# Kernel tuning notes

Hardware: AMD Instinct MI355X
Metric: run time of the kernel (lower is better)

## Reference

```python
import jax, jax.numpy as jnp
import numpy as np

B, T, F = 8192, 30, 16
H1, H2 = 64, 32


def _lstm(x, Wih, Whh, b):
    """PyTorch-convention LSTM (gate order i,f,g,o). x: [B,T,I] -> (ys [B,T,H], hT [B,H])."""
    H = Whh.shape[1]
    h0 = jnp.zeros((x.shape[0], H), x.dtype)

    def step(carry, xt):
        h, c = carry
        z = xt @ Wih.T + h @ Whh.T + b  # [B,4H]
        i, f, g, o = jnp.split(z, 4, axis=-1)
        c = jax.nn.sigmoid(f) * c + jax.nn.sigmoid(i) * jnp.tanh(g)
        h = jax.nn.sigmoid(o) * jnp.tanh(c)
        return (h, c), h

    (hT, _), ys = jax.lax.scan(step, (h0, h0), jnp.swapaxes(x, 0, 1))
    return jnp.swapaxes(ys, 0, 1), hT


def setup_inputs() -> dict:
    key = jax.random.key(0)
    ks = jax.random.split(key, 16)
    s = 0.1  # small init scale for numerical sanity
    return {
        "x": jax.random.normal(ks[0], (B, T, F), jnp.float32),
        "Wih1": jax.random.normal(ks[1], (4 * H1, F), jnp.float32) * s,
        "Whh1": jax.random.normal(ks[2], (4 * H1, H1), jnp.float32) * s,
        "b1": jax.random.normal(ks[3], (4 * H1,), jnp.float32) * s,
        "Wih2": jax.random.normal(ks[4], (4 * H2, H1), jnp.float32) * s,
        "Whh2": jax.random.normal(ks[5], (4 * H2, H2), jnp.float32) * s,
        "b2": jax.random.normal(ks[6], (4 * H2,), jnp.float32) * s,
        "Wih3": jax.random.normal(ks[7], (4 * H2, H2), jnp.float32) * s,
        "Whh3": jax.random.normal(ks[8], (4 * H2, H2), jnp.float32) * s,
        "b3": jax.random.normal(ks[9], (4 * H2,), jnp.float32) * s,
        "Wih4": jax.random.normal(ks[10], (4 * H1, H2), jnp.float32) * s,
        "Whh4": jax.random.normal(ks[11], (4 * H1, H1), jnp.float32) * s,
        "b4": jax.random.normal(ks[12], (4 * H1,), jnp.float32) * s,
        "Wout": jax.random.normal(ks[13], (F, H1), jnp.float32) * s,
        "bout": jax.random.normal(ks[14], (F,), jnp.float32) * s,
    }


def reference(x, Wih1, Whh1, b1, Wih2, Whh2, b2, Wih3, Whh3, b3, Wih4, Whh4, b4, Wout, bout):
    ys1, _ = _lstm(x, Wih1, Whh1, b1)          # encoder LSTM(64)
    _, latent = _lstm(ys1, Wih2, Whh2, b2)      # encoder LSTM(32) -> final hidden [B,32]
    repeated = jnp.broadcast_to(latent[:, None, :], (latent.shape[0], T, latent.shape[1]))
    ys3, _ = _lstm(repeated, Wih3, Whh3, b3)    # decoder LSTM(32)
    ys4, _ = _lstm(ys3, Wih4, Whh4, b4)         # decoder LSTM(64)
    return ys4 @ Wout.T + bout                  # [B,T,F]
```

## Files before the change

### kernel.cpp

```cpp
#include <hip/hip_runtime.h>


#define TT 30
#define FF 16
#define NT 768

typedef unsigned short u16t;
typedef __attribute__((ext_vector_type(8))) short short8;
typedef __attribute__((ext_vector_type(4))) short short4v;
typedef __attribute__((ext_vector_type(4))) float floatx4;

#define MFMA(a, b, c) __builtin_amdgcn_mfma_f32_16x16x32_bf16(a, b, c, 0, 0, 0)

#if __has_builtin(__builtin_amdgcn_exp2f)
#define EXP2(x) __builtin_amdgcn_exp2f(x)
#else
#define EXP2(x) exp2f(x)
#endif

template <int P> struct IC { static constexpr int v = P; };

__device__ __forceinline__ float rcpf(float v) { return __builtin_amdgcn_rcpf(v); }
__device__ __forceinline__ u16t f2bf(float f) {
  unsigned int u = __float_as_uint(f);
  u = (u + 0x7FFFu + ((u >> 16) & 1u)) >> 16;
  return (u16t)u;
}
__device__ __forceinline__ unsigned int pkbf(float a, float b) {
  unsigned int r;
  asm("v_cvt_pk_bf16_f32 %0, %1, %2" : "=v"(r) : "v"(a), "v"(b));
  return r;
}
__device__ __forceinline__ void barLDS() {
  asm volatile("s_waitcnt lgkmcnt(0)" ::: "memory");
  __builtin_amdgcn_s_barrier();
}
__device__ __forceinline__ short8 ldFragS(const float* p, float s) {
  const float4 lo = *(const float4*)p;
  const float4 hi = *(const float4*)(p + 4);
  short8 r;
  r[0] = (short)f2bf(lo.x * s); r[1] = (short)f2bf(lo.y * s);
  r[2] = (short)f2bf(lo.z * s); r[3] = (short)f2bf(lo.w * s);
  r[4] = (short)f2bf(hi.x * s); r[5] = (short)f2bf(hi.y * s);
  r[6] = (short)f2bf(hi.z * s); r[7] = (short)f2bf(hi.w * s);
  return r;
}
__device__ __forceinline__ float cellUp(const floatx4 acc, float& c) {
  float ei = EXP2(-acc[0]);
  float ef = EXP2(-acc[1]);
  float eg = EXP2(-acc[2]);
  float eo = EXP2(-acc[3]);
  float pig = (1.f + ei) * (1.f + eg);
  float pf  = 1.f + ef;
  float num = c * pig + (1.f - eg) * pf;
  c = num * rcpf(pf * pig);
  float ec = EXP2(-2.885390082f * c);
  return (1.f - ec) * rcpf((1.f + eo) * (1.f + ec));
}

__global__ __launch_bounds__(NT, 3) void lstm_ae_mfma12(
    const float* __restrict__ x,
    const float* __restrict__ Wih1, const float* __restrict__ Whh1, const float* __restrict__ b1,
    const float* __restrict__ Wih2, const float* __restrict__ Whh2, const float* __restrict__ b2,
    const float* __restrict__ Wih3, const float* __restrict__ Whh3, const float* __restrict__ b3,
    const float* __restrict__ Wih4, const float* __restrict__ Whh4, const float* __restrict__ b4,
    const float* __restrict__ Wout, const float* __restrict__ bout,
    float* __restrict__ out)
{
  __shared__ __align__(16) u16t xAll[32 * 968];
  __shared__ __align__(16) u16t aB[32 * 264];

  const int t = threadIdx.x;
  const int w = t >> 6, lane = t & 63;
  const int q = lane >> 4, n = lane & 15;
  const int q8 = q * 8;
  const int bBase = blockIdx.x * 32;
  const int nlo = n >> 2, ngt = n & 3;
  const bool isZ1 = (w < 8);
  const int hf = w & 1;
  const int jA = w >> 1;
  const int j2 = (w >> 1) - 4;
  const int rh = (n + 16 * hf) * 264;
  const int xh = (n + 16 * hf) * 968;

  const float L1 = 1.442695041f, L2 = 2.885390082f;
  const float sA = (ngt == 2) ? L2 : L1;

  for (int i = t; i < 32 * 264; i += NT) aB[i] = 0;
  {
    const float* xb = x + (size_t)bBase * (TT * FF);
    for (int i4 = t; i4 < 3840; i4 += NT) {
      int e = i4 * 4;
      int b = e / 480, r = e - b * 480;
      int stp = r >> 4, f = r & 15;
      float4 v = *(const float4*)&xb[e];
      short4v s4 = { (short)f2bf(v.x), (short)f2bf(v.y), (short)f2bf(v.z), (short)f2bf(v.w) };
      *(short4v*)&xAll[b * 968 + stp * 32 + f] = s4;
    }
    for (int i = t; i < 15360; i += NT) {
      int b = i / 480, r = i - b * 480;
      int stp = r >> 4, f = r & 15;
      xAll[b * 968 + stp * 32 + 16 + f] = 0;
    }
  }
  const short8 z8 = { 0, 0, 0, 0, 0, 0, 0, 0 };
  short8 wAf[4][3]; floatx4 biasA[4];
  if (isZ1) {
#pragma unroll
    for (int tt = 0; tt < 4; ++tt) {
      int T = jA + 4 * tt;
      int row = ngt * 64 + T * 4 + nlo;
      wAf[tt][0] = z8;
      if (q < 2) wAf[tt][0] = ldFragS(&Wih1[row * 16 + q8], sA);
      wAf[tt][1] = ldFragS(&Whh1[row * 64 + q8], sA);
      wAf[tt][2] = ldFragS(&Whh1[row * 64 + 32 + q8], sA);
#pragma unroll
      for (int r = 0; r < 4; ++r) biasA[tt][r] = b1[r * 64 + T * 4 + q] * (r == 2 ? L2 : L1);
    }
  } else {
#pragma unroll
    for (int tt = 0; tt < 4; ++tt) {
      int T = j2 + 2 * tt;
      int row = ngt * 32 + T * 4 + nlo;
      wAf[tt][0] = ldFragS(&Wih2[row * 64 + q8], sA);
      wAf[tt][1] = ldFragS(&Wih2[row * 64 + 32 + q8], sA);
      wAf[tt][2] = ldFragS(&Whh2[row * 32 + q8], sA);
#pragma unroll
      for (int r = 0; r < 4; ++r) biasA[tt][r] = b2[r * 32 + T * 4 + q] * (r == 2 ? L2 : L1);
    }
  }
  __syncthreads();

  float cA[4] = {0.f, 0.f, 0.f, 0.f};
  short8 bxN;
  float hv[4];

  if (isZ1) {
    const short8 bx0 = *(const short8*)&xAll[xh + q8];
#pragma unroll
    for (int tt = 0; tt < 4; ++tt) {
      floatx4 a = biasA[tt];
      a = MFMA(wAf[tt][0], bx0, a);
      hv[tt] = cellUp(a, cA[tt]);
    }
    unsigned int pk01 = pkbf(hv[0], hv[1]);
    unsigned int pk23 = pkbf(hv[2], hv[3]);
    aB[rh + (jA + 0) * 4 + q] = (u16t)pk01;
    aB[rh + (jA + 4) * 4 + q] = (u16t)(pk01 >> 16);
    aB[rh + (jA + 8) * 4 + q] = (u16t)pk23;
    aB[rh + (jA + 12) * 4 + q] = (u16t)(pk23 >> 16);
    bxN = *(const short8*)&xAll[xh + 32 + q8];
  }
  barLDS();

  auto stepA = [&](int st, auto pc) {
    constexpr int p = decltype(pc)::v;
    const short8 h1a = *(const short8*)&aB[rh + p * 64 + q8];
    const short8 h1b = *(const short8*)&aB[rh + p * 64 + 32 + q8];
    if (isZ1) {
#pragma unroll
      for (int tt = 0; tt < 4; ++tt) {
        floatx4 a = biasA[tt];
        a = MFMA(wAf[tt][0], bxN, a);
        a = MFMA(wAf[tt][1], h1a, a);
        a = MFMA(wAf[tt][2], h1b, a);
        hv[tt] = cellUp(a, cA[tt]);
      }
      unsigned int pk01 = pkbf(hv[0], hv[1]);
      unsigned int pk23 = pkbf(hv[2], hv[3]);
      aB[rh + (1 - p) * 64 + (jA + 0) * 4 + q] = (u16t)pk01;
      aB[rh + (1 - p) * 64 + (jA + 4) * 4 + q] = (u16t)(pk01 >> 16);
      aB[rh + (1 - p) * 64 + (jA + 8) * 4 + q] = (u16t)pk23;
      aB[rh + (1 - p) * 64 + (jA + 12) * 4 + q] = (u16t)(pk23 >> 16);
      const int nx = (st + 2 < TT) ? st + 2 : TT - 1;
      bxN = *(const short8*)&xAll[xh + nx * 32 + q8];
    } else {
      const short8 h2 = *(const short8*)&aB[rh + 128 + (1 - p) * 32 + q8];
#pragma unroll
      for (int tt = 0; tt < 4; ++tt) {
        floatx4 a = biasA[tt];
        a = MFMA(wAf[tt][0], h1a, a);
        a = MFMA(wAf[tt][1], h1b, a);
        a = MFMA(wAf[tt][2], h2, a);
        hv[tt] = cellUp(a, cA[tt]);
      }
      unsigned int pk01 = pkbf(hv[0], hv[1]);
      unsigned int pk23 = pkbf(hv[2], hv[3]);
      aB[rh + 128 + p * 32 + (j2 + 0) * 4 + q] = (u16t)pk01;
      aB[rh + 128 + p * 32 + (j2 + 2) * 4 + q] = (u16t)(pk01 >> 16);
      aB[rh + 128 + p * 32 + (j2 + 4) * 4 + q] = (u16t)pk23;
      aB[rh + 128 + p * 32 + (j2 + 6) * 4 + q] = (u16t)(pk23 >> 16);
    }
    barLDS();
  };
  for (int st = 0; st < 28; st += 2) { stepA(st, IC<0>{}); stepA(st + 1, IC<1>{}); }
  stepA(28, IC<0>{});
  if (!isZ1) {
    const short8 h1a = *(const short8*)&aB[rh + 64 + q8];
    const short8 h1b = *(const short8*)&aB[rh + 96 + q8];
    const short8 h2  = *(const short8*)&aB[rh + 128 + q8];
#pragma unroll
    for (int tt = 0; tt < 4; ++tt) {
      floatx4 a = biasA[tt];
      a = MFMA(wAf[tt][0], h1a, a);
      a = MFMA(wAf[tt][1], h1b, a);
      a = MFMA(wAf[tt][2], h2, a);
      hv[tt] = cellUp(a, cA[tt]);
    }
    unsigned int pk01 = pkbf(hv[0], hv[1]);
    unsigned int pk23 = pkbf(hv[2], hv[3]);
    aB[rh + 160 + (j2 + 0) * 4 + q] = (u16t)pk01;
    aB[rh + 160 + (j2 + 2) * 4 + q] = (u16t)(pk01 >> 16);
    aB[rh + 160 + (j2 + 4) * 4 + q] = (u16t)pk23;
    aB[rh + 160 + (j2 + 6) * 4 + q] = (u16t)(pk23 >> 16);
  }
  __syncthreads();

  short8 wBf[4][3]; floatx4 biasB[4];
  short8 wof[2]; floatx4 biasO;
  short8 w3h[4]; floatx4 acc3c[4];
  if (isZ1) {
#pragma unroll
    for (int tt = 0; tt < 4; ++tt) {
      int T = jA + 4 * tt;
      int row = ngt * 64 + T * 4 + nlo;
      wBf[tt][0] = ldFragS(&Wih4[row * 32 + q8], sA);
      wBf[tt][1] = ldFragS(&Whh4[row * 64 + q8], sA);
      wBf[tt][2] = ldFragS(&Whh4[row * 64 + 32 + q8], sA);
#pragma unroll
      for (int r = 0; r < 4; ++r) biasB[tt][r] = b4[r * 64 + T * 4 + q] * (r == 2 ? L2 : L1);
    }
    wof[0] = ldFragS(&Wout[n * 64 + q8], 1.f);
    wof[1] = ldFragS(&Wout[n * 64 + 32 + q8], 1.f);
    biasO = *(const floatx4*)&bout[q * 4];
  } else {
    const short8 blat = *(const short8*)&aB[rh + 160 + q8];
#pragma unroll
    for (int tt = 0; tt < 4; ++tt) {
      int T = j2 + 2 * tt;
      int row = ngt * 32 + T * 4 + nlo;
      const short8 w3i = ldFragS(&Wih3[row * 32 + q8], sA);
      w3h[tt] = ldFragS(&Whh3[row * 32 + q8], sA);
      floatx4 b3v;
#pragma unroll
      for (int r = 0; r < 4; ++r) b3v[r] = b3[r * 32 + T * 4 + q] * (r == 2 ? L2 : L1);
      acc3c[tt] = MFMA(w3i, blat, b3v);
    }
  }
  for (int i = t; i < 2048; i += NT) aB[(i >> 6) * 264 + 64 + (i & 63)] = 0;
  __syncthreads();

  float cB[4] = {0.f, 0.f, 0.f, 0.f};

  if (!isZ1) {
#pragma unroll
    for (int tt = 0; tt < 4; ++tt) hv[tt] = cellUp(acc3c[tt], cB[tt]);
    unsigned int pk01 = pkbf(hv[0], hv[1]);
    unsigned int pk23 = pkbf(hv[2], hv[3]);
    aB[rh + 192 + (j2 + 0) * 4 + q] = (u16t)pk01;
    aB[rh + 192 + (j2 + 2) * 4 + q] = (u16t)(pk01 >> 16);
    aB[rh + 192 + (j2 + 4) * 4 + q] = (u16t)pk23;
    aB[rh + 192 + (j2 + 6) * 4 + q] = (u16t)(pk23 >> 16);
  }
  barLDS();

  auto stepB = [&](int st, auto pc) {
    constexpr int p = decltype(pc)::v;
    const short8 h3 = *(const short8*)&aB[rh + 192 + p * 32 + q8];
    if (isZ1) {
      const short8 h4a = *(const short8*)&aB[rh + (1 - p) * 64 + q8];
      const short8 h4b = *(const short8*)&aB[rh + (1 - p) * 64 + 32 + q8];
#pragma unroll
      for (int tt = 0; tt < 4; ++tt) {
        floatx4 a = biasB[tt];
        a = MFMA(wBf[tt][0], h3, a);
        a = MFMA(wBf[tt][1], h4a, a);
        a = MFMA(wBf[tt][2], h4b, a);
        hv[tt] = cellUp(a, cB[tt]);
      }
      unsigned int pk01 = pkbf(hv[0], hv[1]);
      unsigned int pk23 = pkbf(hv[2], hv[3]);
      aB[rh + p * 64 + (jA + 0) * 4 + q] = (u16t)pk01;
      aB[rh + p * 64 + (jA + 4) * 4 + q] = (u16t)(pk01 >> 16);
      aB[rh + p * 64 + (jA + 8) * 4 + q] = (u16t)pk23;
      aB[rh + p * 64 + (jA + 12) * 4 + q] = (u16t)(pk23 >> 16);
      if (st > 0 && jA == ((st - 1) & 3)) {
        floatx4 y = biasO;
        y = MFMA(wof[0], h4a, y);
        y = MFMA(wof[1], h4b, y);
        *(floatx4*)&out[((size_t)(bBase + n + 16 * hf) * TT + (st - 1)) * FF + q * 4] = y;
      }
    } else {
#pragma unroll
      for (int tt = 0; tt < 4; ++tt) {
        floatx4 a = MFMA(w3h[tt], h3, acc3c[tt]);
        hv[tt] = cellUp(a, cB[tt]);
      }
      unsigned int pk01 = pkbf(hv[0], hv[1]);
      unsigned int pk23 = pkbf(hv[2], hv[3]);
      aB[rh + 192 + (1 - p) * 32 + (j2 + 0) * 4 + q] = (u16t)pk01;
      aB[rh + 192 + (1 - p) * 32 + (j2 + 2) * 4 + q] = (u16t)(pk01 >> 16);
      aB[rh + 192 + (1 - p) * 32 + (j2 + 4) * 4 + q] = (u16t)pk23;
      aB[rh + 192 + (1 - p) * 32 + (j2 + 6) * 4 + q] = (u16t)(pk23 >> 16);
    }
    barLDS();
  };
  for (int st = 0; st < 28; st += 2) { stepB(st, IC<0>{}); stepB(st + 1, IC<1>{}); }
  stepB(28, IC<0>{});
  if (isZ1) {
    const short8 h3  = *(const short8*)&aB[rh + 224 + q8];
    const short8 h4a = *(const short8*)&aB[rh + q8];
    const short8 h4b = *(const short8*)&aB[rh + 32 + q8];
#pragma unroll
    for (int tt = 0; tt < 4; ++tt) {
      floatx4 a = biasB[tt];
      a = MFMA(wBf[tt][0], h3, a);
      a = MFMA(wBf[tt][1], h4a, a);
      a = MFMA(wBf[tt][2], h4b, a);
      hv[tt] = cellUp(a, cB[tt]);
    }
    unsigned int pk01 = pkbf(hv[0], hv[1]);
    unsigned int pk23 = pkbf(hv[2], hv[3]);
    aB[rh + 64 + (jA + 0) * 4 + q] = (u16t)pk01;
    aB[rh + 64 + (jA + 4) * 4 + q] = (u16t)(pk01 >> 16);
    aB[rh + 64 + (jA + 8) * 4 + q] = (u16t)pk23;
    aB[rh + 64 + (jA + 12) * 4 + q] = (u16t)(pk23 >> 16);
    if (jA == 0) {
      floatx4 y = biasO;
      y = MFMA(wof[0], h4a, y);
      y = MFMA(wof[1], h4b, y);
      *(floatx4*)&out[((size_t)(bBase + n + 16 * hf) * TT + 28) * FF + q * 4] = y;
    }
  }
  barLDS();
  if (isZ1 && jA == 1) {
    const short8 ba = *(const short8*)&aB[rh + 64 + q8];
    const short8 bb = *(const short8*)&aB[rh + 96 + q8];
    floatx4 y = biasO;
    y = MFMA(wof[0], ba, y);
    y = MFMA(wof[1], bb, y);
    *(floatx4*)&out[((size_t)(bBase + n + 16 * hf) * TT + 29) * FF + q * 4] = y;
  }
}

extern "C" void kernel_launch(void* const* d_in, const int* in_sizes, int n_in,
                              void* d_out, int out_size, void* d_ws, size_t ws_size,
                              hipStream_t stream) {
  const float* x    = (const float*)d_in[0];
  const float* Wih1 = (const float*)d_in[1];
  const float* Whh1 = (const float*)d_in[2];
  const float* b1   = (const float*)d_in[3];
  const float* Wih2 = (const float*)d_in[4];
  const float* Whh2 = (const float*)d_in[5];
  const float* b2   = (const float*)d_in[6];
  const float* Wih3 = (const float*)d_in[7];
  const float* Whh3 = (const float*)d_in[8];
  const float* b3   = (const float*)d_in[9];
  const float* Wih4 = (const float*)d_in[10];
  const float* Whh4 = (const float*)d_in[11];
  const float* b4   = (const float*)d_in[12];
  const float* Wout = (const float*)d_in[13];
  const float* bout = (const float*)d_in[14];
  float* out = (float*)d_out;

  const int B = in_sizes[0] / (TT * FF);
  dim3 grid(B / 32), block(NT);
  lstm_ae_mfma12<<<grid, block, 0, stream>>>(
      x, Wih1, Whh1, b1, Wih2, Whh2, b2, Wih3, Whh3, b3,
      Wih4, Whh4, b4, Wout, bout, out);
}
```

Before: 161.4 us.

## Replace block-wide barriers with per-half LDS flag synchronization between LSTM waves

Swaps each per-timestep block barrier for LDS flag counters. A wave spins on only the flags of the producer waves it depends on, within its own 16-row batch half. Wave-to-work assignment is regrouped so each half's layer-1/layer-2 (and layer-3/layer-4) waves form independent groups that can drift out of lockstep. The aim is to cut barrier stalls and let the two stacked layers pipeline across timesteps. It adds spin-polling overhead and relies on LDS ordering with volatile flags, which carries a memory-ordering risk. Double buffers can race if a consumer lags more than one step behind.

```diff
diff --git a/kernel.cpp b/kernel.cpp
--- a/kernel.cpp
+++ b/kernel.cpp
@@ -30,10 +30,6 @@
   unsigned int r;
   asm("v_cvt_pk_bf16_f32 %0, %1, %2" : "=v"(r) : "v"(a), "v"(b));
   return r;
-}
-__device__ __forceinline__ void barLDS() {
-  asm volatile("s_waitcnt lgkmcnt(0)" ::: "memory");
-  __builtin_amdgcn_s_barrier();
 }
 __device__ __forceinline__ short8 ldFragS(const float* p, float s) {
   const float4 lo = *(const float4*)p;
@@ -57,8 +53,26 @@
   float ec = EXP2(-2.885390082f * c);
   return (1.f - ec) * rcpf((1.f + eo) * (1.f + ec));
 }
-
-__global__ __launch_bounds__(NT, 3) void lstm_ae_mfma12(
+__device__ __forceinline__ void wait4(const int* f, int tgt) {
+  for (;;) {
+    int a = *(volatile const int*)&f[0];
+    int b = *(volatile const int*)&f[1];
+    int c = *(volatile const int*)&f[2];
+    int d = *(volatile const int*)&f[3];
+    if (a >= tgt && b >= tgt && c >= tgt && d >= tgt) break;
+    __builtin_amdgcn_s_sleep(1);
+  }
+}
+__device__ __forceinline__ void wait2(const int* f, int tgt) {
+  for (;;) {
+    int a = *(volatile const int*)&f[0];
+    int b = *(volatile const int*)&f[1];
+    if (a >= tgt && b >= tgt) break;
+    __builtin_amdgcn_s_sleep(1);
+  }
+}
+
+__global__ __launch_bounds__(NT, 3) void lstm_ae_mfma13(
     const float* __restrict__ x,
     const float* __restrict__ Wih1, const float* __restrict__ Whh1, const float* __restrict__ b1,
     const float* __restrict__ Wih2, const float* __restrict__ Whh2, const float* __restrict__ b2,
@@ -69,6 +83,7 @@
 {
   __shared__ __align__(16) u16t xAll[32 * 968];
   __shared__ __align__(16) u16t aB[32 * 264];
+  __shared__ int flg[16];
 
   const int t = threadIdx.x;
   const int w = t >> 6, lane = t & 63;
@@ -77,16 +92,18 @@
   const int bBase = blockIdx.x * 32;
   const int nlo = n >> 2, ngt = n & 3;
   const bool isZ1 = (w < 8);
-  const int hf = w & 1;
-  const int jA = w >> 1;
-  const int j2 = (w >> 1) - 4;
+  const int hf = isZ1 ? ((w >> 2) & 1) : (w & 1);
+  const int jA = w & 3;
+  const int j2 = (w >> 1) & 1;
   const int rh = (n + 16 * hf) * 264;
   const int xh = (n + 16 * hf) * 968;
+  const int myFlag = isZ1 ? (hf * 4 + jA) : (8 + hf * 2 + j2);
 
   const float L1 = 1.442695041f, L2 = 2.885390082f;
   const float sA = (ngt == 2) ? L2 : L1;
 
   for (int i = t; i < 32 * 264; i += NT) aB[i] = 0;
+  for (int i = t; i < 16; i += NT) flg[i] = -1;
   {
     const float* xb = x + (size_t)bBase * (TT * FF);
     for (int i4 = t; i4 < 3840; i4 += NT) {
@@ -132,73 +149,41 @@
   __syncthreads();
 
   float cA[4] = {0.f, 0.f, 0.f, 0.f};
-  short8 bxN;
   float hv[4];
 
-  if (isZ1) {
-    const short8 bx0 = *(const short8*)&xAll[xh + q8];
+  auto stepA1 = [&](int s, auto pc) {
+    constexpr int P = pc.v;
+    wait4(&flg[hf * 4], s - 1);
+    wait2(&flg[8 + hf * 2], s - 2);
+    __builtin_amdgcn_sched_barrier(0);
+    const short8 bx  = *(const short8*)&xAll[xh + s * 32 + q8];
+    const short8 h1a = *(const short8*)&aB[rh + (1 - P) * 64 + q8];
+    const short8 h1b = *(const short8*)&aB[rh + (1 - P) * 64 + 32 + q8];
 #pragma unroll
     for (int tt = 0; tt < 4; ++tt) {
       floatx4 a = biasA[tt];
-      a = MFMA(wAf[tt][0], bx0, a);
+      a = MFMA(wAf[tt][0], bx, a);
+      a = MFMA(wAf[tt][1], h1a, a);
+      a = MFMA(wAf[tt][2], h1b, a);
       hv[tt] = cellUp(a, cA[tt]);
     }
     unsigned int pk01 = pkbf(hv[0], hv[1]);
     unsigned int pk23 = pkbf(hv[2], hv[3]);
-    aB[rh + (jA + 0) * 4 + q] = (u16t)pk01;
-    aB[rh + (jA + 4) * 4 + q] = (u16t)(pk01 >> 16);
-    aB[rh + (jA + 8) * 4 + q] = (u16t)pk23;
-    aB[rh + (jA + 12) * 4 + q] = (u16t)(pk23 >> 16);
-    bxN = *(const short8*)&xAll[xh + 32 + q8];
-  }
-  barLDS();
-
-  auto stepA = [&](int st, auto pc) {
-    constexpr int p = decltype(pc)::v;
-    const short8 h1a = *(const short8*)&aB[rh + p * 64 + q8];
-    const short8 h1b = *(const short8*)&aB[rh + p * 64 + 32 + q8];
-    if (isZ1) {
-#pragma unroll
-      for (int tt = 0; tt < 4; ++tt) {
-        floatx4 a = biasA[tt];
-        a = MFMA(wAf[tt][0], bxN, a);
-        a = MFMA(wAf[tt][1], h1a, a);
-        a = MFMA(wAf[tt][2], h1b, a);
-        hv[tt] = cellUp(a, cA[tt]);
-      }
-      unsigned int pk01 = pkbf(hv[0], hv[1]);
-      unsigned int pk23 = pkbf(hv[2], hv[3]);
-      aB[rh + (1 - p) * 64 + (jA + 0) * 4 + q] = (u16t)pk01;
-      aB[rh + (1 - p) * 64 + (jA + 4) * 4 + q] = (u16t)(pk01 >> 16);
-      aB[rh + (1 - p) * 64 + (jA + 8) * 4 + q] = (u16t)pk23;
-      aB[rh + (1 - p) * 64 + (jA + 12) * 4 + q] = (u16t)(pk23 >> 16);
-      const int nx = (st + 2 < TT) ? st + 2 : TT - 1;
-      bxN = *(const short8*)&xAll[xh + nx * 32 + q8];
-    } else {
-      const short8 h2 = *(const short8*)&aB[rh + 128 + (1 - p) * 32 + q8];
-#pragma unroll
-      for (int tt = 0; tt < 4; ++tt) {
-        floatx4 a = biasA[tt];
-        a = MFMA(wAf[tt][0], h1a, a);
-        a = MFMA(wAf[tt][1], h1b, a);
-        a = MFMA(wAf[tt][2], h2, a);
-        hv[tt] = cellUp(a, cA[tt]);
-      }
-      unsigned int pk01 = pkbf(hv[0], hv[1]);
-      unsigned int pk23 = pkbf(hv[2], hv[3]);
-      aB[rh + 128 + p * 32 + (j2 + 0) * 4 + q] = (u16t)pk01;
-      aB[rh + 128 + p * 32 + (j2 + 2) * 4 + q] = (u16t)(pk01 >> 16);
-      aB[rh + 128 + p * 32 + (j2 + 4) * 4 + q] = (u16t)pk23;
-      aB[rh + 128 + p * 32 + (j2 + 6) * 4 + q] = (u16t)(pk23 >> 16);
-    }
-    barLDS();
+    aB[rh + P * 64 + (jA + 0) * 4 + q] = (u16t)pk01;
+    aB[rh + P * 64 + (jA + 4) * 4 + q] = (u16t)(pk01 >> 16);
+    aB[rh + P * 64 + (jA + 8) * 4 + q] = (u16t)pk23;
+    aB[rh + P * 64 + (jA + 12) * 4 + q] = (u16t)(pk23 >> 16);
+    asm volatile("s_waitcnt lgkmcnt(0)" ::: "memory");
+    *(volatile int*)&flg[myFlag] = s;
   };
-  for (int st = 0; st < 28; st += 2) { stepA(st, IC<0>{}); stepA(st + 1, IC<1>{}); }
-  stepA(28, IC<0>{});
-  if (!isZ1) {
-    const short8 h1a = *(const short8*)&aB[rh + 64 + q8];
-    const short8 h1b = *(const short8*)&aB[rh + 96 + q8];
-    const short8 h2  = *(const short8*)&aB[rh + 128 + q8];
+  auto stepA2 = [&](int s, auto pc) {
+    constexpr int P = pc.v;
+    wait4(&flg[hf * 4], s);
+    wait2(&flg[8 + hf * 2], s - 1);
+    __builtin_amdgcn_sched_barrier(0);
+    const short8 h1a = *(const short8*)&aB[rh + P * 64 + q8];
+    const short8 h1b = *(const short8*)&aB[rh + P * 64 + 32 + q8];
+    const short8 h2  = *(const short8*)&aB[rh + 128 + (1 - P) * 32 + q8];
 #pragma unroll
     for (int tt = 0; tt < 4; ++tt) {
       floatx4 a = biasA[tt];
@@ -209,13 +194,23 @@
     }
     unsigned int pk01 = pkbf(hv[0], hv[1]);
     unsigned int pk23 = pkbf(hv[2], hv[3]);
-    aB[rh + 160 + (j2 + 0) * 4 + q] = (u16t)pk01;
-    aB[rh + 160 + (j2 + 2) * 4 + q] = (u16t)(pk01 >> 16);
-    aB[rh + 160 + (j2 + 4) * 4 + q] = (u16t)pk23;
-    aB[rh + 160 + (j2 + 6) * 4 + q] = (u16t)(pk23 >> 16);
+    const int base = (s == TT - 1) ? (rh + 160) : (rh + 128 + P * 32);
+    aB[base + (j2 + 0) * 4 + q] = (u16t)pk01;
+    aB[base + (j2 + 2) * 4 + q] = (u16t)(pk01 >> 16);
+    aB[base + (j2 + 4) * 4 + q] = (u16t)pk23;
+    aB[base + (j2 + 6) * 4 + q] = (u16t)(pk23 >> 16);
+    asm volatile("s_waitcnt lgkmcnt(0)" ::: "memory");
+    *(volatile int*)&flg[myFlag] = s;
+  };
+  if (isZ1) {
+    for (int s = 0; s < TT; s += 2) { stepA1(s, IC<0>{}); stepA1(s + 1, IC<1>{}); }
+  } else {
+    for (int s = 0; s < TT; s += 2) { stepA2(s, IC<0>{}); stepA2(s + 1, IC<1>{}); }
   }
   __syncthreads();
 
+  for (int i = t; i < 16; i += NT) flg[i] = -1;
+  for (int i = t; i < 2048; i += NT) aB[(i >> 6) * 264 + 64 + (i & 63)] = 0;
   short8 wBf[4][3]; floatx4 biasB[4];
   short8 wof[2]; floatx4 biasO;
   short8 w3h[4]; floatx4 acc3c[4];
@@ -247,70 +242,18 @@
       acc3c[tt] = MFMA(w3i, blat, b3v);
     }
   }
-  for (int i = t; i < 2048; i += NT) aB[(i >> 6) * 264 + 64 + (i & 63)] = 0;
   __syncthreads();
 
   float cB[4] = {0.f, 0.f, 0.f, 0.f};
 
-  if (!isZ1) {
-#pragma unroll
-    for (int tt = 0; tt < 4; ++tt) hv[tt] = cellUp(acc3c[tt], cB[tt]);
-    unsigned int pk01 = pkbf(hv[0], hv[1]);
-    unsigned int pk23 = pkbf(hv[2], hv[3]);
-    aB[rh + 192 + (j2 + 0) * 4 + q] = (u16t)pk01;
-    aB[rh + 192 + (j2 + 2) * 4 + q] = (u16t)(pk01 >> 16);
-    aB[rh + 192 + (j2 + 4) * 4 + q] = (u16t)pk23;
-    aB[rh + 192 + (j2 + 6) * 4 + q] = (u16t)(pk23 >> 16);
-  }
-  barLDS();
-
-  auto stepB = [&](int st, auto pc) {
-    constexpr int p = decltype(pc)::v;
-    const short8 h3 = *(const short8*)&aB[rh + 192 + p * 32 + q8];
-    if (isZ1) {
-      const short8 h4a = *(const short8*)&aB[rh + (1 - p) * 64 + q8];
-      const short8 h4b = *(const short8*)&aB[rh + (1 - p) * 64 + 32 + q8];
-#pragma unroll
-      for (int tt = 0; tt < 4; ++tt) {
-        floatx4 a = biasB[tt];
-        a = MFMA(wBf[tt][0], h3, a);
-        a = MFMA(wBf[tt][1], h4a, a);
-        a = MFMA(wBf[tt][2], h4b, a);
-        hv[tt] = cellUp(a, cB[tt]);
-      }
-      unsigned int pk01 = pkbf(hv[0], hv[1]);
-      unsigned int pk23 = pkbf(hv[2], hv[3]);
-      aB[rh + p * 64 + (jA + 0) * 4 + q] = (u16t)pk01;
-      aB[rh + p * 64 + (jA + 4) * 4 + q] = (u16t)(pk01 >> 16);
-      aB[rh + p * 64 + (jA + 8) * 4 + q] = (u16t)pk23;
-      aB[rh + p * 64 + (jA + 12) * 4 + q] = (u16t)(pk23 >> 16);
-      if (st > 0 && jA == ((st - 1) & 3)) {
-        floatx4 y = biasO;
-        y = MFMA(wof[0], h4a, y);
-        y = MFMA(wof[1], h4b, y);
-        *(floatx4*)&out[((size_t)(bBase + n + 16 * hf) * TT + (st - 1)) * FF + q * 4] = y;
-      }
-    } else {
-#pragma unroll
-      for (int tt = 0; tt < 4; ++tt) {
-        floatx4 a = MFMA(w3h[tt], h3, acc3c[tt]);
-        hv[tt] = cellUp(a, cB[tt]);
-      }
-      unsigned int pk01 = pkbf(hv[0], hv[1]);
-      unsigned int pk23 = pkbf(hv[2], hv[3]);
-      aB[rh + 192 + (1 - p) * 32 + (j2 + 0) * 4 + q] = (u16t)pk01;
-      aB[rh + 192 + (1 - p) * 32 + (j2 + 2) * 4 + q] = (u16t)(pk01 >> 16);
-      aB[rh + 192 + (1 - p) * 32 + (j2 + 4) * 4 + q] = (u16t)pk23;
-      aB[rh + 192 + (1 - p) * 32 + (j2 + 6) * 4 + q] = (u16t)(pk23 >> 16);
-    }
-    barLDS();
-  };
-  for (int st = 0; st < 28; st += 2) { stepB(st, IC<0>{}); stepB(st + 1, IC<1>{}); }
-  stepB(28, IC<0>{});
-  if (isZ1) {
-    const short8 h3  = *(const short8*)&aB[rh + 224 + q8];
-    const short8 h4a = *(const short8*)&aB[rh + q8];
-    const short8 h4b = *(const short8*)&aB[rh + 32 + q8];
+  auto stepB4 = [&](int s, auto pc) {
+    constexpr int P = pc.v;
+    wait2(&flg[8 + hf * 2], s);
+    wait4(&flg[hf * 4], s - 1);
+    __builtin_amdgcn_sched_barrier(0);
+    const short8 h3  = *(const short8*)&aB[rh + 192 + P * 32 + q8];
+    const short8 h4a = *(const short8*)&aB[rh + (1 - P) * 64 + q8];
+    const short8 h4b = *(const short8*)&aB[rh + (1 - P) * 64 + 32 + q8];
 #pragma unroll
     for (int tt = 0; tt < 4; ++tt) {
       floatx4 a = biasB[tt];
@@ -321,25 +264,53 @@
     }
     unsigned int pk01 = pkbf(hv[0], hv[1]);
     unsigned int pk23 = pkbf(hv[2], hv[3]);
-    aB[rh + 64 + (jA + 0) * 4 + q] = (u16t)pk01;
-    aB[rh + 64 + (jA + 4) * 4 + q] = (u16t)(pk01 >> 16);
-    aB[rh + 64 + (jA + 8) * 4 + q] = (u16t)pk23;
-    aB[rh + 64 + (jA + 12) * 4 + q] = (u16t)(pk23 >> 16);
-    if (jA == 0) {
+    aB[rh + P * 64 + (jA + 0) * 4 + q] = (u16t)pk01;
+    aB[rh + P * 64 + (jA + 4) * 4 + q] = (u16t)(pk01 >> 16);
+    aB[rh + P * 64 + (jA + 8) * 4 + q] = (u16t)pk23;
+    aB[rh + P * 64 + (jA + 12) * 4 + q] = (u16t)(pk23 >> 16);
+    asm volatile("s_waitcnt lgkmcnt(0)" ::: "memory");
+    *(volatile int*)&flg[myFlag] = s;
+    if (s > 0 && jA == ((s - 1) & 3)) {
       floatx4 y = biasO;
       y = MFMA(wof[0], h4a, y);
       y = MFMA(wof[1], h4b, y);
-      *(floatx4*)&out[((size_t)(bBase + n + 16 * hf) * TT + 28) * FF + q * 4] = y;
-    }
-  }
-  barLDS();
-  if (isZ1 && jA == 1) {
-    const short8 ba = *(const short8*)&aB[rh + 64 + q8];
-    const short8 bb = *(const short8*)&aB[rh + 96 + q8];
-    floatx4 y = biasO;
-    y = MFMA(wof[0], ba, y);
-    y = MFMA(wof[1], bb, y);
-    *(floatx4*)&out[((size_t)(bBase + n + 16 * hf) * TT + 29) * FF + q * 4] = y;
+      *(floatx4*)&out[((size_t)(bBase + n + 16 * hf) * TT + (s - 1)) * FF + q * 4] = y;
+    }
+  };
+  auto stepB3 = [&](int s, auto pc) {
+    constexpr int P = pc.v;
+    wait2(&flg[8 + hf * 2], s - 1);
+    wait4(&flg[hf * 4], s - 2);
+    __builtin_amdgcn_sched_barrier(0);
+    const short8 h3p = *(const short8*)&aB[rh + 192 + (1 - P) * 32 + q8];
+#pragma unroll
+    for (int tt = 0; tt < 4; ++tt) {
+      floatx4 a = MFMA(w3h[tt], h3p, acc3c[tt]);
+      hv[tt] = cellUp(a, cB[tt]);
+    }
+    unsigned int pk01 = pkbf(hv[0], hv[1]);
+    unsigned int pk23 = pkbf(hv[2], hv[3]);
+    aB[rh + 192 + P * 32 + (j2 + 0) * 4 + q] = (u16t)pk01;
+    aB[rh + 192 + P * 32 + (j2 + 2) * 4 + q] = (u16t)(pk01 >> 16);
+    aB[rh + 192 + P * 32 + (j2 + 4) * 4 + q] = (u16t)pk23;
+    aB[rh + 192 + P * 32 + (j2 + 6) * 4 + q] = (u16t)(pk23 >> 16);
+    asm volatile("s_waitcnt lgkmcnt(0)" ::: "memory");
+    *(volatile int*)&flg[myFlag] = s;
+  };
+  if (isZ1) {
+    for (int s = 0; s < TT; s += 2) { stepB4(s, IC<0>{}); stepB4(s + 1, IC<1>{}); }
+    if (jA == 1) {
+      wait4(&flg[hf * 4], TT - 1);
+      __builtin_amdgcn_sched_barrier(0);
+      const short8 ba = *(const short8*)&aB[rh + 64 + q8];
+      const short8 bb = *(const short8*)&aB[rh + 96 + q8];
+      floatx4 y = biasO;
+      y = MFMA(wof[0], ba, y);
+      y = MFMA(wof[1], bb, y);
+      *(floatx4*)&out[((size_t)(bBase + n + 16 * hf) * TT + (TT - 1)) * FF + q * 4] = y;
+    }
+  } else {
+    for (int s = 0; s < TT; s += 2) { stepB3(s, IC<0>{}); stepB3(s + 1, IC<1>{}); }
   }
 }
 
@@ -365,7 +336,7 @@
 
   const int B = in_sizes[0] / (TT * FF);
   dim3 grid(B / 32), block(NT);
-  lstm_ae_mfma12<<<grid, block, 0, stream>>>(
+  lstm_ae_mfma13<<<grid, block, 0, stream>>>(
       x, Wih1, Whh1, b1, Wih2, Whh2, b2, Wih3, Whh3, b3,
       Wih4, Whh4, b4, Wout, bout, out);
 }
```

Result: slower. 172.3 us (+6.7%).
